# Kernel tuning notes

Measured on AMD Instinct MI355X. Metric: run time of the kernel, lower is better.

## Reference

```python
import jax, jax.numpy as jnp
import numpy as np
from jax import lax

DIM = 256
WS = 8            # window side -> N = 64
H = 8             # num_heads
HD = DIM // H     # head dim = 32
NREF = 30
RB = 4            # reference batch
NWIN = 144        # windows per image (96x96 / 8x8)
N = WS * WS
B_ = RB * NWIN
SCALE = HD ** -0.5
LN_EPS = 1e-5


def make_rel_index():
    coords = np.stack(np.meshgrid(np.arange(WS), np.arange(WS), indexing='ij'))  # (2,WS,WS)
    cf = coords.reshape(2, -1)
    rel = (cf[:, :, None] - cf[:, None, :]).transpose(1, 2, 0).astype(np.int64)
    rel[..., 0] += WS - 1
    rel[..., 1] += WS - 1
    rel[..., 0] *= 2 * WS - 1
    return jnp.asarray(rel.sum(-1), jnp.int32)  # (N, N)


def setup_inputs() -> dict:
    key = jax.random.key(0)
    ks = jax.random.split(key, 10)
    return {
        'x': jax.random.normal(ks[0], (B_, N, DIM), jnp.float32),
        'mask': jnp.zeros((NWIN, N, N), jnp.float32),
        'x_ref': jax.random.normal(ks[1], (RB, DIM, NREF), jnp.float32),
        'qkv_w': jax.random.normal(ks[2], (3 * DIM, DIM), jnp.float32) * 0.02,
        'qkv_b': jnp.zeros((3 * DIM,), jnp.float32),
        'proj_w': jax.random.normal(ks[3], (DIM, DIM), jnp.float32) * 0.02,
        'proj_b': jnp.zeros((DIM,), jnp.float32),
        'bias_table': jax.random.normal(ks[4], ((2 * WS - 1) ** 2, H), jnp.float32) * 0.02,
        'diff_mu': jax.random.normal(ks[5], (1, 1, DIM), jnp.float32),
        'diff_logsigma': jax.random.normal(ks[6], (1, 1, DIM), jnp.float32) * 0.05,
        'ref_qk_w': jax.random.normal(ks[7], (2 * NREF, NREF), jnp.float32) * 0.1,
        'ref_qk_b': jnp.zeros((2 * NREF,), jnp.float32),
        'conv_w': jax.random.normal(ks[8], (H, H, 3, 3), jnp.float32) * 0.05,
        'conv_b': jnp.zeros((H,), jnp.float32),
        'rel_index': make_rel_index(),
    }


def _layer_norm_2d(a):
    # layer norm over the last two dims, no affine (F.layer_norm(x, [n_win*N, n_rf]))
    m = jnp.mean(a, axis=(-2, -1), keepdims=True)
    v = jnp.var(a, axis=(-2, -1), keepdims=True)
    return (a - m) * lax.rsqrt(v + LN_EPS)


def reference(x, mask, x_ref, qkv_w, qkv_b, proj_w, proj_b, bias_table,
              diff_mu, diff_logsigma, ref_qk_w, ref_qk_b, conv_w, conv_b, rel_index):
    # qkv projection -> (3, B_, H, N, HD)
    qkv = (x @ qkv_w.T + qkv_b).reshape(B_, N, 3, H, HD).transpose(2, 0, 3, 1, 4)
    q, k, v = qkv[0], qkv[1], qkv[2]

    # reference queries/values: x_ref (RB, DIM, NREF) -> (RB, 2*NREF, DIM)
    ref = (x_ref @ ref_qk_w.T + ref_qk_b).transpose(0, 2, 1)
    ref_q = diff_mu + jnp.exp(diff_logsigma) * ref[:, :NREF]   # (RB, NREF, DIM)
    ref_q = ref_q.reshape(RB, NREF, H, HD).transpose(0, 2, 1, 3)       # (RB, H, NREF, HD)
    ref_v = ref[:, NREF:].reshape(RB, NREF, H, HD).transpose(0, 2, 1, 3)

    # cross-attn scores q @ ref_k^T, broadcast ref over windows of the same batch
    qb = q.reshape(RB, NWIN, H, N, HD)
    ref_attn = jnp.einsum('bwhnd,bhrd->bhwnr', qb, ref_q)  # (RB, H, NWIN, N, NREF)
    ref_attn = ref_attn.reshape(RB, H, NWIN * N, NREF)

    # 3-step conv diffusion refinement with layernorm+gelu residual
    for _ in range(3):
        upd = lax.conv_general_dilated(
            ref_attn, conv_w, window_strides=(1, 1), padding=((1, 1), (1, 1)),
            dimension_numbers=('NCHW', 'OIHW', 'NCHW')) + conv_b[None, :, None, None]
        ref_attn = ref_attn + jax.nn.gelu(_layer_norm_2d(upd), approximate=False)

    ref_attn = ref_attn.reshape(RB, H, NWIN, N, NREF).transpose(0, 2, 1, 3, 4)  # (RB,NWIN,H,N,NREF)
    ref_attn = jax.nn.softmax(ref_attn, axis=-1)
    q_new = jnp.einsum('bwhnr,bhrd->bwhnd', ref_attn, ref_v) * SCALE

    # window attention with relative position bias + mask
    attn = jnp.einsum('bwhnd,bwhmd->bwhnm', q_new, k.reshape(RB, NWIN, H, N, HD))
    rel_bias = bias_table[rel_index.reshape(-1)].reshape(N, N, H).transpose(2, 0, 1)  # (H,N,N)
    attn = attn + rel_bias[None, None] + mask[None, :, None]
    attn = jax.nn.softmax(attn, axis=-1)

    out = jnp.einsum('bwhnm,bwhmd->bwhnd', attn, v.reshape(RB, NWIN, H, N, HD))
    out = out.transpose(0, 1, 3, 2, 4).reshape(B_, N, DIM)
    return out @ proj_w.T + proj_b
```

## Files before the change

### kernel.cpp

```cpp
#include <hip/hip_runtime.h>
#include <math.h>

#define NHD 8
#define HD 32
#define NREF 30
#define RB 4
#define NWIN 144
#define NTOK 64
#define IMG_H (NWIN*NTOK)
#define LN_CNT (IMG_H*NREF)
#define SCALE 0.1767766952966369f
#define LN_EPS 1e-5f

typedef __attribute__((ext_vector_type(8))) short bf8_t;
typedef __attribute__((ext_vector_type(4))) float f4_t;

__device__ __forceinline__ float gelu_f(float v) {
    return 0.5f * v * (1.0f + erff(v * 0.7071067811865476f));
}

__device__ __forceinline__ short f2bf(float f) {
    union { float f; unsigned u; } v; v.f = f;
    unsigned r = v.u + 0x7fffu + ((v.u >> 16) & 1u);
    return (short)(r >> 16);
}

__device__ __forceinline__ float bf2f(unsigned short u) {
    union { unsigned u; float f; } v; v.u = ((unsigned)u) << 16;
    return v.f;
}

__global__ __launch_bounds__(256) void k_cvt(
    const float* __restrict__ src, unsigned short* __restrict__ dst, int n8) {
    const int stride = gridDim.x * blockDim.x;
    for (int i = blockIdx.x * blockDim.x + threadIdx.x; i < n8; i += stride) {
        const float* s = src + (size_t)i * 8;
        float4 a = *reinterpret_cast<const float4*>(s);
        float4 b = *reinterpret_cast<const float4*>(s + 4);
        bf8_t p;
        p[0] = f2bf(a.x); p[1] = f2bf(a.y); p[2] = f2bf(a.z); p[3] = f2bf(a.w);
        p[4] = f2bf(b.x); p[5] = f2bf(b.y); p[6] = f2bf(b.z); p[7] = f2bf(b.w);
        *reinterpret_cast<bf8_t*>(dst + (size_t)i * 8) = p;
    }
}

__global__ __launch_bounds__(256) void k_refprep(
    const float* __restrict__ x_ref, const float* __restrict__ rw,
    const float* __restrict__ rbias, const float* __restrict__ dmu,
    const float* __restrict__ dls, float* __restrict__ ref_q,
    float* __restrict__ ref_v) {
    __shared__ float Wl[60][NREF];
    __shared__ float Bl[60];
    const int rb = blockIdx.x;
    const int t = threadIdx.x;
    for (int i = t; i < 60 * NREF; i += 256) Wl[i / NREF][i % NREF] = rw[i];
    if (t < 60) Bl[t] = rbias[t];
    __syncthreads();
    const int d = t;
    float xr[NREF];
#pragma unroll
    for (int r = 0; r < NREF; ++r) xr[r] = x_ref[(rb * 256 + d) * NREF + r];
    const int h = d >> 5, hd = d & 31;
    const float mu = dmu[d], sg = expf(dls[d]);
    for (int j = 0; j < 60; ++j) {
        float acc = Bl[j];
#pragma unroll
        for (int r = 0; r < NREF; ++r) acc += xr[r] * Wl[j][r];
        if (j < NREF)
            ref_q[((rb * NHD + h) * NREF + j) * HD + hd] = mu + sg * acc;
        else
            ref_v[((rb * NHD + h) * NREF + (j - NREF)) * HD + hd] = acc;
    }
}

__global__ __launch_bounds__(256) void k_bm(
    const float* __restrict__ mask, const float* __restrict__ bias_table,
    const int* __restrict__ rel_index, float* __restrict__ bmt) {
    const int wh = blockIdx.x;
    const int w = wh >> 3, h = wh & 7;
    for (int u = threadIdx.x; u < 4096; u += 256) {
        const int m = u >> 6, n = u & 63;
        bmt[(size_t)wh * 4096 + u] = mask[(size_t)w * 4096 + n * 64 + m]
                                   + bias_table[rel_index[n * 64 + m] * NHD + h];
    }
}

__global__ __launch_bounds__(256) void k_qkv_mfma(
    const unsigned short* __restrict__ xb, const unsigned short* __restrict__ wb,
    const float* __restrict__ bias, unsigned short* __restrict__ qb,
    unsigned short* __restrict__ kb, unsigned short* __restrict__ vb) {
    __shared__ __align__(16) char As[64 * 512];
    __shared__ __align__(16) char Bs[64 * 512];
    const int t = threadIdx.x;
    const int bid = blockIdx.x;
    const int swz = (bid & 7) * (6912 / 8) + (bid >> 3);
    const int r0 = (swz / 12) * 64;
    const int c0 = (swz % 12) * 64;
#pragma unroll
    for (int i = 0; i < 8; ++i) {
        const int c = t + 256 * i;
        const int row = c >> 5, k8 = c & 31;
        bf8_t pa = *reinterpret_cast<const bf8_t*>(&xb[(size_t)(r0 + row) * 256 + k8 * 8]);
        *reinterpret_cast<bf8_t*>(As + row * 512 + ((k8 * 16) ^ ((row & 7) << 4))) = pa;
        bf8_t pb = *reinterpret_cast<const bf8_t*>(&wb[(size_t)(c0 + row) * 256 + k8 * 8]);
        *reinterpret_cast<bf8_t*>(Bs + row * 512 + ((k8 * 16) ^ ((row & 7) << 4))) = pb;
    }
    __syncthreads();
    const int wid = t >> 6, l = t & 63;
    const int wr = wid >> 1, wc = wid & 1;
    const int lr = l & 15, lg = l >> 4;
    const int sw = (lr & 7) << 4;
    const char* Ap0 = As + (wr * 32 + lr) * 512;
    const char* Ap1 = As + (wr * 32 + 16 + lr) * 512;
    const char* Bp0 = Bs + (wc * 32 + lr) * 512;
    const char* Bp1 = Bs + (wc * 32 + 16 + lr) * 512;
    f4_t acc[2][2] = {};
#pragma unroll
    for (int kk = 0; kk < 8; ++kk) {
        const int ka = (kk * 64 + lg * 16) ^ sw;
        bf8_t a0 = *reinterpret_cast<const bf8_t*>(Ap0 + ka);
        bf8_t a1 = *reinterpret_cast<const bf8_t*>(Ap1 + ka);
        bf8_t b0 = *reinterpret_cast<const bf8_t*>(Bp0 + ka);
        bf8_t b1 = *reinterpret_cast<const bf8_t*>(Bp1 + ka);
        acc[0][0] = __builtin_amdgcn_mfma_f32_16x16x32_bf16(a0, b0, acc[0][0], 0, 0, 0);
        acc[0][1] = __builtin_amdgcn_mfma_f32_16x16x32_bf16(a0, b1, acc[0][1], 0, 0, 0);
        acc[1][0] = __builtin_amdgcn_mfma_f32_16x16x32_bf16(a1, b0, acc[1][0], 0, 0, 0);
        acc[1][1] = __builtin_amdgcn_mfma_f32_16x16x32_bf16(a1, b1, acc[1][1], 0, 0, 0);
    }
#pragma unroll
    for (int ni = 0; ni < 2; ++ni) {
        const int gc = c0 + wc * 32 + ni * 16 + lr;
        const int i3 = gc >> 8, rem = gc & 255;
        const int h = rem >> 5, hd = rem & 31;
        const float bv = bias[gc];
        unsigned short* dst = (i3 == 0) ? qb : (i3 == 1) ? kb : vb;
#pragma unroll
        for (int mi = 0; mi < 2; ++mi)
#pragma unroll
            for (int j = 0; j < 4; ++j) {
                const int gr = r0 + wr * 32 + mi * 16 + lg * 4 + j;
                const int bb = gr >> 6, n = gr & 63;
                dst[(size_t)((bb * NHD + h) * NTOK + n) * HD + hd] =
                    (unsigned short)f2bf(acc[mi][ni][j] + bv);
            }
    }
}

__global__ __launch_bounds__(256) void k_proj_mfma(
    const unsigned short* __restrict__ A, const unsigned short* __restrict__ w,
    const float* __restrict__ bias, float* __restrict__ out) {
    __shared__ __align__(16) char As[64 * 512];
    __shared__ __align__(16) char Bs[64 * 512];
    const int t = threadIdx.x;
    const int bid = blockIdx.x;
    const int swz = (bid & 7) * (2304 / 8) + (bid >> 3);
    const int r0 = (swz / 4) * 64;
    const int c0 = (swz % 4) * 64;
#pragma unroll
    for (int i = 0; i < 8; ++i) {
        const int c = t + 256 * i;
        const int row = c >> 5, k8 = c & 31;
        bf8_t pa = *reinterpret_cast<const bf8_t*>(&A[(size_t)(r0 + row) * 256 + k8 * 8]);
        *reinterpret_cast<bf8_t*>(As + row * 512 + ((k8 * 16) ^ ((row & 7) << 4))) = pa;
        bf8_t pb = *reinterpret_cast<const bf8_t*>(&w[(size_t)(c0 + row) * 256 + k8 * 8]);
        *reinterpret_cast<bf8_t*>(Bs + row * 512 + ((k8 * 16) ^ ((row & 7) << 4))) = pb;
    }
    __syncthreads();
    const int wid = t >> 6, l = t & 63;
    const int wr = wid >> 1, wc = wid & 1;
    const int lr = l & 15, lg = l >> 4;
    const int sw = (lr & 7) << 4;
    const char* Ap0 = As + (wr * 32 + lr) * 512;
    const char* Ap1 = As + (wr * 32 + 16 + lr) * 512;
    const char* Bp0 = Bs + (wc * 32 + lr) * 512;
    const char* Bp1 = Bs + (wc * 32 + 16 + lr) * 512;
    f4_t acc[2][2] = {};
#pragma unroll
    for (int kk = 0; kk < 8; ++kk) {
        const int ka = (kk * 64 + lg * 16) ^ sw;
        bf8_t a0 = *reinterpret_cast<const bf8_t*>(Ap0 + ka);
        bf8_t a1 = *reinterpret_cast<const bf8_t*>(Ap1 + ka);
        bf8_t b0 = *reinterpret_cast<const bf8_t*>(Bp0 + ka);
        bf8_t b1 = *reinterpret_cast<const bf8_t*>(Bp1 + ka);
        acc[0][0] = __builtin_amdgcn_mfma_f32_16x16x32_bf16(a0, b0, acc[0][0], 0, 0, 0);
        acc[0][1] = __builtin_amdgcn_mfma_f32_16x16x32_bf16(a0, b1, acc[0][1], 0, 0, 0);
        acc[1][0] = __builtin_amdgcn_mfma_f32_16x16x32_bf16(a1, b0, acc[1][0], 0, 0, 0);
        acc[1][1] = __builtin_amdgcn_mfma_f32_16x16x32_bf16(a1, b1, acc[1][1], 0, 0, 0);
    }
#pragma unroll
    for (int ni = 0; ni < 2; ++ni) {
        const int gc = c0 + wc * 32 + ni * 16 + lr;
        const float bv = bias[gc];
#pragma unroll
        for (int mi = 0; mi < 2; ++mi) {
#pragma unroll
            for (int j = 0; j < 4; ++j) {
                const int gr = r0 + wr * 32 + mi * 16 + lg * 4 + j;
                out[(size_t)gr * 256 + gc] = acc[mi][ni][j] + bv;
            }
        }
    }
}

__global__ __launch_bounds__(256) void k_scores(
    const unsigned short* __restrict__ qbuf, const float* __restrict__ ref_q,
    float* __restrict__ scores) {
    const int bid = blockIdx.x;
    const int wg = bid % 36;
    const int rh = bid / 36;
    const int h = rh % NHD, rb = rh / NHD;
    __shared__ __align__(16) float rs[NREF][32];
    __shared__ float outb[4][64 * NREF];
    const int t = threadIdx.x;
    const int wv = t >> 6, n = t & 63;
    const float* rsrc = &ref_q[(size_t)rh * NREF * HD];
    for (int u = t; u < NREF * 8; u += 256) {
        const int row = u >> 3, c4 = u & 7;
        *reinterpret_cast<float4*>(&rs[row][c4 * 4]) =
            *reinterpret_cast<const float4*>(&rsrc[u * 4]);
    }
    __syncthreads();
    const int w = wg * 4 + wv;
    const unsigned short* qsrc = &qbuf[(size_t)((rb * NWIN + w) * NHD + h) * NTOK * HD + n * 32];
    float q[32];
#pragma unroll
    for (int c8 = 0; c8 < 4; ++c8) {
        bf8_t v = *reinterpret_cast<const bf8_t*>(&qsrc[c8 * 8]);
#pragma unroll
        for (int j = 0; j < 8; ++j)
            q[c8 * 8 + j] = bf2f((unsigned short)v[j]);
    }
    for (int r = 0; r < NREF; ++r) {
        float acc = 0.f;
#pragma unroll
        for (int d = 0; d < 32; ++d) acc += q[d] * rs[r][d];
        outb[wv][n * NREF + r] = acc;
    }
    float* dst = &scores[(size_t)((rb * NHD + h) * IMG_H + w * 64) * NREF];
    for (int u = n; u < 64 * NREF; u += 64) dst[u] = outb[wv][u];
}

template<int FUSED>
__global__ __launch_bounds__(256) void k_conv_mfma(
    const float* __restrict__ scPrev, const unsigned short* __restrict__ updPrev,
    const float* __restrict__ stPrev, const float* __restrict__ conv_w,
    const float* __restrict__ conv_b, float* __restrict__ scOut,
    unsigned short* __restrict__ updOut, float* __restrict__ stats) {
    const int bid = blockIdx.x;
    const int rb = bid / 288;
    const int y0 = (bid % 288) * 32;
    __shared__ __align__(16) unsigned short At[34][32][8];
    __shared__ float red[4][8][2];
    __shared__ float lmean[8], lrsig[8];
    const int t = threadIdx.x;
    if (FUSED) {
        if (t < 8) {
            const float s0 = stPrev[(rb * NHD + t) * 2];
            const float s1 = stPrev[(rb * NHD + t) * 2 + 1];
            const float m = s0 * (1.f / LN_CNT);
            const float v = s1 * (1.f / LN_CNT) - m * m;
            lmean[t] = m;
            lrsig[t] = rsqrtf(v + LN_EPS);
        }
        __syncthreads();
    }
    for (int f = t; f < 34 * 2; f += 256) {
        const int yy = f >> 1, side = (f & 1) ? 31 : 0;
        bf8_t z;
#pragma unroll
        for (int j = 0; j < 8; ++j) z[j] = 0;
        *reinterpret_cast<bf8_t*>(&At[yy][side][0]) = z;
    }
    for (int ps = t; ps < 34 * 30; ps += 256) {
        const int yy = ps / 30, xc = ps % 30;
        const int y = y0 - 1 + yy;
        bf8_t pk;
#pragma unroll
        for (int j = 0; j < 8; ++j) pk[j] = 0;
        if (y >= 0 && y < IMG_H) {
#pragma unroll
            for (int ci = 0; ci < 8; ++ci) {
                const size_t idx = (size_t)((rb * NHD + ci) * IMG_H + y) * NREF + xc;
                float val;
                if (FUSED) {
                    const float u = bf2f(updPrev[idx]);
                    val = scPrev[idx] + gelu_f((u - lmean[ci]) * lrsig[ci]);
                    if (yy >= 1 && yy <= 32) scOut[idx] = val;
                } else {
                    val = scPrev[idx];
                }
                pk[ci] = f2bf(val);
            }
        }
        *reinterpret_cast<bf8_t*>(&At[yy][xc + 1][0]) = pk;
    }
    const int l = t & 63, wv = t >> 6;
    const int lr = l & 15, lg = l >> 4;
    bf8_t wf[3];
#pragma unroll
    for (int kg = 0; kg < 3; ++kg) {
        const int tap = kg * 4 + lg;
        bf8_t wq;
#pragma unroll
        for (int j = 0; j < 8; ++j) wq[j] = 0;
        if (lr < 8 && tap < 9) {
            const int dy = tap / 3, dx = tap % 3;
#pragma unroll
            for (int ci = 0; ci < 8; ++ci)
                wq[ci] = f2bf(conv_w[lr * 72 + ci * 9 + dy * 3 + dx]);
        }
        wf[kg] = wq;
    }
    const float cb = (lr < 8) ? conv_b[lr] : 0.f;
    __syncthreads();
    float ls = 0.f, lss = 0.f;
#pragma unroll 1
    for (int ti = 0; ti < 15; ++ti) {
        const int tile = wv * 15 + ti;
        const int pA = tile * 16 + lr;
        const int ylA = pA / 30, xA = pA % 30;
        f4_t o;
        o[0] = cb; o[1] = cb; o[2] = cb; o[3] = cb;
#pragma unroll
        for (int kg = 0; kg < 3; ++kg) {
            const int tap = kg * 4 + lg;
            const int dy = (tap < 9) ? tap / 3 : 0;
            const int dx = (tap < 9) ? tap % 3 : 0;
            bf8_t a = *reinterpret_cast<const bf8_t*>(&At[ylA + dy][xA + dx][0]);
            o = __builtin_amdgcn_mfma_f32_16x16x32_bf16(a, wf[kg], o, 0, 0, 0);
        }
        if (lr < 8) {
#pragma unroll
            for (int j = 0; j < 4; ++j) {
                const int pD = tile * 16 + lg * 4 + j;
                const int yl = pD / 30, x = pD % 30;
                updOut[(size_t)((rb * NHD + lr) * IMG_H + y0 + yl) * NREF + x] =
                    (unsigned short)f2bf(o[j]);
                ls += o[j];
                lss += o[j] * o[j];
            }
        }
    }
    ls += __shfl_xor(ls, 16); ls += __shfl_xor(ls, 32);
    lss += __shfl_xor(lss, 16); lss += __shfl_xor(lss, 32);
    if (l < 8) { red[wv][l][0] = ls; red[wv][l][1] = lss; }
    __syncthreads();
    if (t < 8) {
        atomicAdd(&stats[(rb * NHD + t) * 2],
                  red[0][t][0] + red[1][t][0] + red[2][t][0] + red[3][t][0]);
        atomicAdd(&stats[(rb * NHD + t) * 2 + 1],
                  red[0][t][1] + red[1][t][1] + red[2][t][1] + red[3][t][1]);
    }
}

__global__ __launch_bounds__(256) void k_qnewf(
    const float* __restrict__ scores, const unsigned short* __restrict__ upd,
    const float* __restrict__ st, const float* __restrict__ ref_v,
    unsigned short* __restrict__ qbuf) {
    const int bid = blockIdx.x;
    const int wg = bid % 36;
    const int rh = bid / 36;
    const int h = rh % NHD, rb = rh / NHD;
    __shared__ __align__(16) float rv[NREF][32];
    __shared__ float sl[4][64 * NREF];
    const int t = threadIdx.x;
    const int wv = t >> 6, n = t & 63;
    const float s0 = st[rh * 2], s1 = st[rh * 2 + 1];
    const float mean = s0 * (1.f / LN_CNT);
    const float var = s1 * (1.f / LN_CNT) - mean * mean;
    const float rsig = rsqrtf(var + LN_EPS);
    const float* rvs = &ref_v[(size_t)rh * NREF * HD];
    for (int u = t; u < NREF * 8; u += 256) {
        const int r = u >> 3, c4 = u & 7;
        *reinterpret_cast<float4*>(&rv[r][c4 * 4]) =
            *reinterpret_cast<const float4*>(&rvs[u * 4]);
    }
    const int w = wg * 4 + wv;
    const size_t base = (size_t)((rb * NHD + h) * IMG_H + w * 64) * NREF;
    for (int u = n; u < 64 * NREF; u += 64) {
        const float uv = bf2f(upd[base + u]);
        sl[wv][u] = scores[base + u] + gelu_f((uv - mean) * rsig);
    }
    __syncthreads();
    float p[NREF];
    float mx = -1e30f;
#pragma unroll
    for (int r = 0; r < NREF; ++r) { p[r] = sl[wv][n * NREF + r]; mx = fmaxf(mx, p[r]); }
    float sum = 0.f;
#pragma unroll
    for (int r = 0; r < NREF; ++r) { p[r] = expf(p[r] - mx); sum += p[r]; }
    const float inv = SCALE / sum;
    float acc[32] = {0.f};
#pragma unroll
    for (int r = 0; r < NREF; ++r) {
        const float pr = p[r] * inv;
#pragma unroll
        for (int d = 0; d < 32; ++d) acc[d] += pr * rv[r][d];
    }
    unsigned short* dst = &qbuf[(size_t)((rb * NWIN + w) * NHD + h) * NTOK * HD + n * 32];
#pragma unroll
    for (int c8 = 0; c8 < 4; ++c8) {
        bf8_t pk;
#pragma unroll
        for (int j = 0; j < 8; ++j) pk[j] = f2bf(acc[c8 * 8 + j]);
        *reinterpret_cast<bf8_t*>(&dst[c8 * 8]) = pk;
    }
}

__global__ __launch_bounds__(256, 4) void k_wattn_mfma(
    const unsigned short* __restrict__ qbuf, const unsigned short* __restrict__ kbuf,
    const unsigned short* __restrict__ vbuf, const float* __restrict__ bmt,
    unsigned short* __restrict__ pre) {
    const int wh = blockIdx.x;
    const int w = wh >> 3, h = wh & 7;
    const int t = threadIdx.x;
    const int rb = t >> 6;
    const int l = t & 63;
    const int lr = l & 15, lg = l >> 4;
    const int b = rb * NWIN + w;
    const int bid = b * NHD + h;
    __shared__ __align__(16) char P[4][64 * 128];

    f4_t acc[4][4];
    const float* bm = &bmt[(size_t)wh * 4096];
#pragma unroll
    for (int mt = 0; mt < 4; ++mt)
#pragma unroll
        for (int nt = 0; nt < 4; ++nt)
#pragma unroll
            for (int j = 0; j < 4; ++j)
                acc[mt][nt][j] = bm[(mt * 16 + lg * 4 + j) * 64 + nt * 16 + lr];

    const unsigned short* kp = &kbuf[(size_t)bid * 2048];
    const unsigned short* qp = &qbuf[(size_t)bid * 2048];
    bf8_t kf[4], qf[4];
#pragma unroll
    for (int mt = 0; mt < 4; ++mt) {
        kf[mt] = *reinterpret_cast<const bf8_t*>(&kp[(mt * 16 + lr) * 32 + lg * 8]);
        qf[mt] = *reinterpret_cast<const bf8_t*>(&qp[(mt * 16 + lr) * 32 + lg * 8]);
    }
#pragma unroll
    for (int mt = 0; mt < 4; ++mt)
#pragma unroll
        for (int nt = 0; nt < 4; ++nt)
            acc[mt][nt] = __builtin_amdgcn_mfma_f32_16x16x32_bf16(kf[mt], qf[nt], acc[mt][nt], 0, 0, 0);

#pragma unroll
    for (int nt = 0; nt < 4; ++nt) {
        float mx = -1e30f;
#pragma unroll
        for (int mt = 0; mt < 4; ++mt)
#pragma unroll
            for (int j = 0; j < 4; ++j) mx = fmaxf(mx, acc[mt][nt][j]);
        mx = fmaxf(mx, __shfl_xor(mx, 16));
        mx = fmaxf(mx, __shfl_xor(mx, 32));
        float s = 0.f;
#pragma unroll
        for (int mt = 0; mt < 4; ++mt)
#pragma unroll
            for (int j = 0; j < 4; ++j) {
                const float e = expf(acc[mt][nt][j] - mx);
                acc[mt][nt][j] = e;
                s += e;
            }
        s += __shfl_xor(s, 16);
        s += __shfl_xor(s, 32);
        const float inv = 1.f / s;
#pragma unroll
        for (int mt = 0; mt < 4; ++mt)
#pragma unroll
            for (int j = 0; j < 4; ++j) acc[mt][nt][j] *= inv;
    }

    const int n7 = (lr & 7) << 4;
    char* Pw = P[rb];
#pragma unroll
    for (int nt = 0; nt < 4; ++nt) {
        const int rowb = (nt * 16 + lr) * 128;
#pragma unroll
        for (int mt = 0; mt < 4; ++mt)
#pragma unroll
            for (int jp = 0; jp < 2; ++jp) {
                const unsigned lo = (unsigned short)f2bf(acc[mt][nt][jp * 2]);
                const unsigned hi = (unsigned short)f2bf(acc[mt][nt][jp * 2 + 1]);
                const int mb = (mt * 16 + lg * 4 + jp * 2) * 2;
                *reinterpret_cast<unsigned*>(&Pw[rowb + (mb ^ n7)]) = lo | (hi << 16);
            }
    }
    __syncthreads();

    const unsigned short* vp = &vbuf[(size_t)bid * 2048];
    bf8_t vf[2][2];
#pragma unroll
    for (int ht = 0; ht < 2; ++ht)
#pragma unroll
        for (int ks = 0; ks < 2; ++ks) {
            bf8_t tv;
#pragma unroll
            for (int j = 0; j < 8; ++j)
                tv[j] = (short)vp[(ks * 32 + lg * 8 + j) * 32 + ht * 16 + lr];
            vf[ht][ks] = tv;
        }

    f4_t o[2][4] = {};
#pragma unroll
    for (int ks = 0; ks < 2; ++ks)
#pragma unroll
        for (int nt = 0; nt < 4; ++nt) {
            const int rowb = (nt * 16 + lr) * 128;
            bf8_t pf = *reinterpret_cast<const bf8_t*>(&Pw[rowb + ((ks * 64 + lg * 16) ^ n7)]);
#pragma unroll
            for (int ht = 0; ht < 2; ++ht)
                o[ht][nt] = __builtin_amdgcn_mfma_f32_16x16x32_bf16(vf[ht][ks], pf, o[ht][nt], 0, 0, 0);
        }

#pragma unroll
    for (int ht = 0; ht < 2; ++ht)
#pragma unroll
        for (int nt = 0; nt < 4; ++nt) {
            ushort4 pk;
            pk.x = (unsigned short)f2bf(o[ht][nt][0]);
            pk.y = (unsigned short)f2bf(o[ht][nt][1]);
            pk.z = (unsigned short)f2bf(o[ht][nt][2]);
            pk.w = (unsigned short)f2bf(o[ht][nt][3]);
            const int n = nt * 16 + lr;
            const int hd = ht * 16 + lg * 4;
            *reinterpret_cast<ushort4*>(&pre[(size_t)(b * 64 + n) * 256 + h * 32 + hd]) = pk;
        }
}

extern "C" void kernel_launch(void* const* d_in, const int* in_sizes, int n_in,
                              void* d_out, int out_size, void* d_ws, size_t ws_size,
                              hipStream_t stream) {
    const float* x          = (const float*)d_in[0];
    const float* mask       = (const float*)d_in[1];
    const float* x_ref      = (const float*)d_in[2];
    const float* qkv_w      = (const float*)d_in[3];
    const float* qkv_b      = (const float*)d_in[4];
    const float* proj_w     = (const float*)d_in[5];
    const float* proj_b     = (const float*)d_in[6];
    const float* bias_table = (const float*)d_in[7];
    const float* diff_mu    = (const float*)d_in[8];
    const float* diff_ls    = (const float*)d_in[9];
    const float* ref_qk_w   = (const float*)d_in[10];
    const float* ref_qk_b   = (const float*)d_in[11];
    const float* conv_w     = (const float*)d_in[12];
    const float* conv_b     = (const float*)d_in[13];
    const int*   rel_index  = (const int*)d_in[14];
    float* out = (float*)d_out;

    unsigned short* xb   = (unsigned short*)d_ws;
    unsigned short* qb16 = xb + 9437184;
    unsigned short* kb16 = qb16 + 9437184;
    unsigned short* vb16 = kb16 + 9437184;
    float* scA           = (float*)(vb16 + 9437184);
    unsigned short* updA = (unsigned short*)(scA + 8847360);
    unsigned short* updB = updA + 8847360;
    float* rq            = (float*)(updB + 8847360);
    float* rv            = rq + 30720;
    float* st            = rv + 30720;
    float* bmt           = st + 192;
    unsigned short* wqb  = (unsigned short*)(bmt + 4718592);
    unsigned short* wpb  = wqb + 196608;
    float* scB           = (float*)d_ws;
    unsigned short* pre  = (unsigned short*)scA;

    k_cvt<<<2048, 256, 0, stream>>>(x, xb, 9437184 / 8);
    k_cvt<<<96, 256, 0, stream>>>(qkv_w, wqb, 196608 / 8);
    k_cvt<<<32, 256, 0, stream>>>(proj_w, wpb, 65536 / 8);
    k_refprep<<<RB, 256, 0, stream>>>(x_ref, ref_qk_w, ref_qk_b, diff_mu, diff_ls, rq, rv);
    k_bm<<<NWIN * NHD, 256, 0, stream>>>(mask, bias_table, rel_index, bmt);
    k_qkv_mfma<<<6912, 256, 0, stream>>>(xb, wqb, qkv_b, qb16, kb16, vb16);
    k_scores<<<RB * NHD * 36, 256, 0, stream>>>(qb16, rq, scA);
    hipMemsetAsync(st, 0, 192 * sizeof(float), stream);
    k_conv_mfma<0><<<RB * 288, 256, 0, stream>>>(scA, updA, st, conv_w, conv_b, scB, updA, st);
    k_conv_mfma<1><<<RB * 288, 256, 0, stream>>>(scA, updA, st, conv_w, conv_b, scB, updB, st + 64);
    k_conv_mfma<1><<<RB * 288, 256, 0, stream>>>(scB, updB, st + 64, conv_w, conv_b, scA, updA, st + 128);
    k_qnewf<<<RB * NHD * 36, 256, 0, stream>>>(scA, updA, st + 128, rv, qb16);
    k_wattn_mfma<<<NWIN * NHD, 256, 0, stream>>>(qb16, kb16, vb16, bmt, pre);
    k_proj_mfma<<<2304, 256, 0, stream>>>(pre, wpb, proj_b, out);
}
```

Measured before the change: 300.0 us.

## Enlarge QKV and projection GEMM tiles to 128x128 with K-split staging

Both MFMA GEMMs move from 64x64 output tiles with the full K=256 held in shared memory to 128x128 tiles with K loaded in four 64-wide chunks. Each wave now computes a 64x64 sub-tile with 4x4 accumulators, and grids shrink to 1728 and 576 blocks. The intent is higher arithmetic intensity per shared-memory load and less redundant global traffic for the A and B operands. In exchange, every K chunk adds a barrier with no double buffering, register use is higher, and the proj grid of 576 blocks gives fewer blocks per CU.

After: 289.3 us. 1.04x faster.

```diff
diff --git a/kernel.cpp b/kernel.cpp
--- a/kernel.cpp
+++ b/kernel.cpp
@@ -89,59 +89,68 @@
     const unsigned short* __restrict__ xb, const unsigned short* __restrict__ wb,
     const float* __restrict__ bias, unsigned short* __restrict__ qb,
     unsigned short* __restrict__ kb, unsigned short* __restrict__ vb) {
-    __shared__ __align__(16) char As[64 * 512];
-    __shared__ __align__(16) char Bs[64 * 512];
+    __shared__ __align__(16) char As[128 * 128];
+    __shared__ __align__(16) char Bs[128 * 128];
     const int t = threadIdx.x;
     const int bid = blockIdx.x;
-    const int swz = (bid & 7) * (6912 / 8) + (bid >> 3);
-    const int r0 = (swz / 12) * 64;
-    const int c0 = (swz % 12) * 64;
-#pragma unroll
-    for (int i = 0; i < 8; ++i) {
-        const int c = t + 256 * i;
-        const int row = c >> 5, k8 = c & 31;
-        bf8_t pa = *reinterpret_cast<const bf8_t*>(&xb[(size_t)(r0 + row) * 256 + k8 * 8]);
-        *reinterpret_cast<bf8_t*>(As + row * 512 + ((k8 * 16) ^ ((row & 7) << 4))) = pa;
-        bf8_t pb = *reinterpret_cast<const bf8_t*>(&wb[(size_t)(c0 + row) * 256 + k8 * 8]);
-        *reinterpret_cast<bf8_t*>(Bs + row * 512 + ((k8 * 16) ^ ((row & 7) << 4))) = pb;
-    }
-    __syncthreads();
+    const int swz = (bid & 7) * (1728 / 8) + (bid >> 3);
+    const int r0 = (swz / 6) * 128;
+    const int c0 = (swz % 6) * 128;
     const int wid = t >> 6, l = t & 63;
     const int wr = wid >> 1, wc = wid & 1;
     const int lr = l & 15, lg = l >> 4;
-    const int sw = (lr & 7) << 4;
-    const char* Ap0 = As + (wr * 32 + lr) * 512;
-    const char* Ap1 = As + (wr * 32 + 16 + lr) * 512;
-    const char* Bp0 = Bs + (wc * 32 + lr) * 512;
-    const char* Bp1 = Bs + (wc * 32 + 16 + lr) * 512;
-    f4_t acc[2][2] = {};
-#pragma unroll
-    for (int kk = 0; kk < 8; ++kk) {
-        const int ka = (kk * 64 + lg * 16) ^ sw;
-        bf8_t a0 = *reinterpret_cast<const bf8_t*>(Ap0 + ka);
-        bf8_t a1 = *reinterpret_cast<const bf8_t*>(Ap1 + ka);
-        bf8_t b0 = *reinterpret_cast<const bf8_t*>(Bp0 + ka);
-        bf8_t b1 = *reinterpret_cast<const bf8_t*>(Bp1 + ka);
-        acc[0][0] = __builtin_amdgcn_mfma_f32_16x16x32_bf16(a0, b0, acc[0][0], 0, 0, 0);
-        acc[0][1] = __builtin_amdgcn_mfma_f32_16x16x32_bf16(a0, b1, acc[0][1], 0, 0, 0);
-        acc[1][0] = __builtin_amdgcn_mfma_f32_16x16x32_bf16(a1, b0, acc[1][0], 0, 0, 0);
-        acc[1][1] = __builtin_amdgcn_mfma_f32_16x16x32_bf16(a1, b1, acc[1][1], 0, 0, 0);
-    }
-#pragma unroll
-    for (int ni = 0; ni < 2; ++ni) {
-        const int gc = c0 + wc * 32 + ni * 16 + lr;
+    f4_t acc[4][4] = {};
+#pragma unroll 1
+    for (int ks = 0; ks < 4; ++ks) {
+        const int k0 = ks * 64;
+        if (ks) __syncthreads();
+#pragma unroll
+        for (int i = 0; i < 4; ++i) {
+            const int u = t + 256 * i;
+            const int row = u >> 3, c8 = u & 7;
+            bf8_t pa = *reinterpret_cast<const bf8_t*>(&xb[(size_t)(r0 + row) * 256 + k0 + c8 * 8]);
+            *reinterpret_cast<bf8_t*>(As + row * 128 + ((c8 * 16) ^ ((row & 7) << 4))) = pa;
+            bf8_t pb = *reinterpret_cast<const bf8_t*>(&wb[(size_t)(c0 + row) * 256 + k0 + c8 * 8]);
+            *reinterpret_cast<bf8_t*>(Bs + row * 128 + ((c8 * 16) ^ ((row & 7) << 4))) = pb;
+        }
+        __syncthreads();
+#pragma unroll
+        for (int kk = 0; kk < 2; ++kk) {
+            bf8_t a[4], b[4];
+#pragma unroll
+            for (int mt = 0; mt < 4; ++mt) {
+                const int row = wr * 64 + mt * 16 + lr;
+                a[mt] = *reinterpret_cast<const bf8_t*>(
+                    As + row * 128 + ((kk * 64 + lg * 16) ^ ((row & 7) << 4)));
+            }
+#pragma unroll
+            for (int nt = 0; nt < 4; ++nt) {
+                const int row = wc * 64 + nt * 16 + lr;
+                b[nt] = *reinterpret_cast<const bf8_t*>(
+                    Bs + row * 128 + ((kk * 64 + lg * 16) ^ ((row & 7) << 4)));
+            }
+#pragma unroll
+            for (int mt = 0; mt < 4; ++mt)
+#pragma unroll
+                for (int nt = 0; nt < 4; ++nt)
+                    acc[mt][nt] = __builtin_amdgcn_mfma_f32_16x16x32_bf16(a[mt], b[nt], acc[mt][nt], 0, 0, 0);
+        }
+    }
+#pragma unroll
+    for (int nt = 0; nt < 4; ++nt) {
+        const int gc = c0 + wc * 64 + nt * 16 + lr;
         const int i3 = gc >> 8, rem = gc & 255;
         const int h = rem >> 5, hd = rem & 31;
         const float bv = bias[gc];
         unsigned short* dst = (i3 == 0) ? qb : (i3 == 1) ? kb : vb;
 #pragma unroll
-        for (int mi = 0; mi < 2; ++mi)
+        for (int mt = 0; mt < 4; ++mt)
 #pragma unroll
             for (int j = 0; j < 4; ++j) {
-                const int gr = r0 + wr * 32 + mi * 16 + lg * 4 + j;
+                const int gr = r0 + wr * 64 + mt * 16 + lg * 4 + j;
                 const int bb = gr >> 6, n = gr & 63;
                 dst[(size_t)((bb * NHD + h) * NTOK + n) * HD + hd] =
-                    (unsigned short)f2bf(acc[mi][ni][j] + bv);
+                    (unsigned short)f2bf(acc[mt][nt][j] + bv);
             }
     }
 }
@@ -149,56 +158,64 @@
 __global__ __launch_bounds__(256) void k_proj_mfma(
     const unsigned short* __restrict__ A, const unsigned short* __restrict__ w,
     const float* __restrict__ bias, float* __restrict__ out) {
-    __shared__ __align__(16) char As[64 * 512];
-    __shared__ __align__(16) char Bs[64 * 512];
+    __shared__ __align__(16) char As[128 * 128];
+    __shared__ __align__(16) char Bs[128 * 128];
     const int t = threadIdx.x;
     const int bid = blockIdx.x;
-    const int swz = (bid & 7) * (2304 / 8) + (bid >> 3);
-    const int r0 = (swz / 4) * 64;
-    const int c0 = (swz % 4) * 64;
-#pragma unroll
-    for (int i = 0; i < 8; ++i) {
-        const int c = t + 256 * i;
-        const int row = c >> 5, k8 = c & 31;
-        bf8_t pa = *reinterpret_cast<const bf8_t*>(&A[(size_t)(r0 + row) * 256 + k8 * 8]);
-        *reinterpret_cast<bf8_t*>(As + row * 512 + ((k8 * 16) ^ ((row & 7) << 4))) = pa;
-        bf8_t pb = *reinterpret_cast<const bf8_t*>(&w[(size_t)(c0 + row) * 256 + k8 * 8]);
-        *reinterpret_cast<bf8_t*>(Bs + row * 512 + ((k8 * 16) ^ ((row & 7) << 4))) = pb;
-    }
-    __syncthreads();
+    const int swz = (bid & 7) * (576 / 8) + (bid >> 3);
+    const int r0 = (swz / 2) * 128;
+    const int c0 = (swz % 2) * 128;
     const int wid = t >> 6, l = t & 63;
     const int wr = wid >> 1, wc = wid & 1;
     const int lr = l & 15, lg = l >> 4;
-    const int sw = (lr & 7) << 4;
-    const char* Ap0 = As + (wr * 32 + lr) * 512;
-    const char* Ap1 = As + (wr * 32 + 16 + lr) * 512;
-    const char* Bp0 = Bs + (wc * 32 + lr) * 512;
-    const char* Bp1 = Bs + (wc * 32 + 16 + lr) * 512;
-    f4_t acc[2][2] = {};
-#pragma unroll
-    for (int kk = 0; kk < 8; ++kk) {
-        const int ka = (kk * 64 + lg * 16) ^ sw;
-        bf8_t a0 = *reinterpret_cast<const bf8_t*>(Ap0 + ka);
-        bf8_t a1 = *reinterpret_cast<const bf8_t*>(Ap1 + ka);
-        bf8_t b0 = *reinterpret_cast<const bf8_t*>(Bp0 + ka);
-        bf8_t b1 = *reinterpret_cast<const bf8_t*>(Bp1 + ka);
-        acc[0][0] = __builtin_amdgcn_mfma_f32_16x16x32_bf16(a0, b0, acc[0][0], 0, 0, 0);
-        acc[0][1] = __builtin_amdgcn_mfma_f32_16x16x32_bf16(a0, b1, acc[0][1], 0, 0, 0);
-        acc[1][0] = __builtin_amdgcn_mfma_f32_16x16x32_bf16(a1, b0, acc[1][0], 0, 0, 0);
-        acc[1][1] = __builtin_amdgcn_mfma_f32_16x16x32_bf16(a1, b1, acc[1][1], 0, 0, 0);
-    }
-#pragma unroll
-    for (int ni = 0; ni < 2; ++ni) {
-        const int gc = c0 + wc * 32 + ni * 16 + lr;
+    f4_t acc[4][4] = {};
+#pragma unroll 1
+    for (int ks = 0; ks < 4; ++ks) {
+        const int k0 = ks * 64;
+        if (ks) __syncthreads();
+#pragma unroll
+        for (int i = 0; i < 4; ++i) {
+            const int u = t + 256 * i;
+            const int row = u >> 3, c8 = u & 7;
+            bf8_t pa = *reinterpret_cast<const bf8_t*>(&A[(size_t)(r0 + row) * 256 + k0 + c8 * 8]);
+            *reinterpret_cast<bf8_t*>(As + row * 128 + ((c8 * 16) ^ ((row & 7) << 4))) = pa;
+            bf8_t pb = *reinterpret_cast<const bf8_t*>(&w[(size_t)(c0 + row) * 256 + k0 + c8 * 8]);
+            *reinterpret_cast<bf8_t*>(Bs + row * 128 + ((c8 * 16) ^ ((row & 7) << 4))) = pb;
+        }
+        __syncthreads();
+#pragma unroll
+        for (int kk = 0; kk < 2; ++kk) {
+            bf8_t a[4], b[4];
+#pragma unroll
+            for (int mt = 0; mt < 4; ++mt) {
+                const int row = wr * 64 + mt * 16 + lr;
+                a[mt] = *reinterpret_cast<const bf8_t*>(
+                    As + row * 128 + ((kk * 64 + lg * 16) ^ ((row & 7) << 4)));
+            }
+#pragma unroll
+            for (int nt = 0; nt < 4; ++nt) {
+                const int row = wc * 64 + nt * 16 + lr;
+                b[nt] = *reinterpret_cast<const bf8_t*>(
+                    Bs + row * 128 + ((kk * 64 + lg * 16) ^ ((row & 7) << 4)));
+            }
+#pragma unroll
+            for (int mt = 0; mt < 4; ++mt)
+#pragma unroll
+                for (int nt = 0; nt < 4; ++nt)
+                    acc[mt][nt] = __builtin_amdgcn_mfma_f32_16x16x32_bf16(a[mt], b[nt], acc[mt][nt], 0, 0, 0);
+        }
+    }
+#pragma unroll
+    for (int nt = 0; nt < 4; ++nt) {
+        const int gc = c0 + wc * 64 + nt * 16 + lr;
         const float bv = bias[gc];
 #pragma unroll
-        for (int mi = 0; mi < 2; ++mi) {
+        for (int mt = 0; mt < 4; ++mt)
 #pragma unroll
             for (int j = 0; j < 4; ++j) {
-                const int gr = r0 + wr * 32 + mi * 16 + lg * 4 + j;
-                out[(size_t)gr * 256 + gc] = acc[mi][ni][j] + bv;
-            }
-        }
+                const int gr = r0 + wr * 64 + mt * 16 + lg * 4 + j;
+                out[(size_t)gr * 256 + gc] = acc[mt][nt][j] + bv;
+            }
     }
 }
 
@@ -570,7 +587,7 @@
     k_cvt<<<32, 256, 0, stream>>>(proj_w, wpb, 65536 / 8);
     k_refprep<<<RB, 256, 0, stream>>>(x_ref, ref_qk_w, ref_qk_b, diff_mu, diff_ls, rq, rv);
     k_bm<<<NWIN * NHD, 256, 0, stream>>>(mask, bias_table, rel_index, bmt);
-    k_qkv_mfma<<<6912, 256, 0, stream>>>(xb, wqb, qkv_b, qb16, kb16, vb16);
+    k_qkv_mfma<<<1728, 256, 0, stream>>>(xb, wqb, qkv_b, qb16, kb16, vb16);
     k_scores<<<RB * NHD * 36, 256, 0, stream>>>(qb16, rq, scA);
     hipMemsetAsync(st, 0, 192 * sizeof(float), stream);
     k_conv_mfma<0><<<RB * 288, 256, 0, stream>>>(scA, updA, st, conv_w, conv_b, scB, updA, st);
@@ -578,5 +595,5 @@
     k_conv_mfma<1><<<RB * 288, 256, 0, stream>>>(scB, updB, st + 64, conv_w, conv_b, scA, updA, st + 128);
     k_qnewf<<<RB * NHD * 36, 256, 0, stream>>>(scA, updA, st + 128, rv, qb16);
     k_wattn_mfma<<<NWIN * NHD, 256, 0, stream>>>(qb16, kb16, vb16, bmt, pre);
-    k_proj_mfma<<<2304, 256, 0, stream>>>(pre, wpb, proj_b, out);
-}
+    k_proj_mfma<<<576, 256, 0, stream>>>(pre, wpb, proj_b, out);
+}
```
